# Performance work log

Hardware: AMD Instinct MI355X
Metric: run time of the kernel (lower is better)

The kernel has to match this reference:

```python
import jax, jax.numpy as jnp
import numpy as np

B, S, D, H = 2, 2048, 1024, 16
DH = D // H
LN_EPS = 1e-12


def setup_inputs() -> dict:
    key = jax.random.key(0)
    ks = jax.random.split(key, 11)
    s = 0.02
    return {
        "hidden_states": jax.random.normal(ks[0], (B, S, D), dtype=jnp.float32),
        "Wq": jax.random.normal(ks[1], (D, D), dtype=jnp.float32) * s,
        "bq": jnp.zeros((D,), jnp.float32),
        "Wk": jax.random.normal(ks[2], (D, D), dtype=jnp.float32) * s,
        "bk": jnp.zeros((D,), jnp.float32),
        "Wv": jax.random.normal(ks[3], (D, D), dtype=jnp.float32) * s,
        "bv": jnp.zeros((D,), jnp.float32),
        "Wd": jax.random.normal(ks[4], (D, D), dtype=jnp.float32) * s,  # torch Linear weight [out,in]
        "bd": jnp.zeros((D,), jnp.float32),
        "ln_g": jnp.ones((D,), jnp.float32),
        "ln_b": jnp.zeros((D,), jnp.float32),
    }


def reference(hidden_states, Wq, bq, Wk, bk, Wv, bv, Wd, bd, ln_g, ln_b):
    x = hidden_states  # [B,S,D]
    # torch Linear: y = x @ W.T + b
    def heads(y):
        return y.reshape(B, S, H, DH).transpose(0, 2, 1, 3)  # [B,H,S,DH]

    q = heads(x @ Wq.T + bq)
    k = heads(x @ Wk.T + bk)
    v = heads(x @ Wv.T + bv)

    scores = jnp.einsum('bhsd,bhtd->bhst', q, k) / jnp.sqrt(jnp.float32(DH))
    probs = jax.nn.softmax(scores, axis=-1)  # [B,H,S,S]
    ctx = jnp.einsum('bhst,bhtd->bshd', probs, v)  # [B,S,H,DH]

    # fused output projection: einsum('bfnd,ndh->bfh') with w = Wd.T reshaped
    w = Wd.T.reshape(H, DH, D)
    proj = jnp.einsum('bfnd,ndh->bfh', ctx, w) + bd  # [B,S,D]

    mu = jnp.mean(proj, axis=-1, keepdims=True)
    var = jnp.var(proj, axis=-1, keepdims=True)
    out = (proj - mu) / jnp.sqrt(var + LN_EPS) * ln_g + ln_b
    return out
```

## Files before the change

### kernel.cpp

```cpp
#include <hip/hip_runtime.h>

#define HD 16
#define DHEAD 64
#define DMODEL 1024
#define BB 2
#define SS 2048
#define MTOT (BB*SS)
#define LOG2E 1.44269504f

typedef float f32x4 __attribute__((ext_vector_type(4)));
typedef float f32x16 __attribute__((ext_vector_type(16)));
typedef __bf16 bf16x8 __attribute__((ext_vector_type(8)));
typedef unsigned short u16x8 __attribute__((ext_vector_type(8)));
typedef unsigned int u32x2 __attribute__((ext_vector_type(2)));
typedef unsigned int u32x4 __attribute__((ext_vector_type(4)));

__device__ __forceinline__ unsigned short f2bf(float f) {
    unsigned int u = __builtin_bit_cast(unsigned int, f);
    unsigned int r = (u + 0x7fffu + ((u >> 16) & 1u)) >> 16;
    return (unsigned short)r;
}

__device__ __forceinline__ bf16x8 ld8(const unsigned short* p) {
    u16x8 v = *reinterpret_cast<const u16x8*>(p);
    return __builtin_bit_cast(bf16x8, v);
}

__device__ __forceinline__ void gload_lds16b(const char* g, char* l) {
    __builtin_amdgcn_global_load_lds(
        (const __attribute__((address_space(1))) void*)g,
        (__attribute__((address_space(3))) void*)l, 16, 0, 0);
}

__device__ __forceinline__ unsigned cvt_pk_bf16(float lo, float hi) {
    unsigned r;
    asm("v_cvt_pk_bf16_f32 %0, %1, %2" : "=v"(r) : "v"(lo), "v"(hi));
    return r;
}

__global__ __launch_bounds__(256) void cvt_all(
    const float* __restrict__ x,
    const float* __restrict__ w0, const float* __restrict__ w1,
    const float* __restrict__ w2, const float* __restrict__ w3,
    unsigned short* __restrict__ xb,
    unsigned short* __restrict__ o0, unsigned short* __restrict__ o1,
    unsigned short* __restrict__ o2, unsigned short* __restrict__ o3) {
    int y = blockIdx.y;
    const float* in;
    unsigned short* out;
    int idx;
    if (y < 4) {
        in  = (y == 0) ? w0 : (y == 1) ? w1 : (y == 2) ? w2 : w3;
        out = (y == 0) ? o0 : (y == 1) ? o1 : (y == 2) ? o2 : o3;
        idx = blockIdx.x * 256 + threadIdx.x;
    } else {
        in  = x;
        out = xb;
        idx = ((y - 4) * 1024 + blockIdx.x) * 256 + threadIdx.x;
    }
    float4 v = reinterpret_cast<const float4*>(in)[idx];
    ushort4 o;
    o.x = f2bf(v.x); o.y = f2bf(v.y); o.z = f2bf(v.z); o.w = f2bf(v.w);
    reinterpret_cast<ushort4*>(out)[idx] = o;
}

__global__ __launch_bounds__(256, 2) void gemm_qkv(
    const unsigned short* __restrict__ xb,
    const unsigned short* __restrict__ Wqb, const unsigned short* __restrict__ Wkb,
    const unsigned short* __restrict__ Wvb,
    const float* __restrict__ bq, const float* __restrict__ bk, const float* __restrict__ bv,
    unsigned short* __restrict__ Qo, unsigned short* __restrict__ Ko, unsigned short* __restrict__ VTo) {
    __shared__ unsigned short Als[2][8192];
    __shared__ unsigned short Bls[2][8192];
    int L = blockIdx.x;
    int wg = (L & 7) * 96 + (L >> 3);
    int z = wg >> 8, rem = wg & 255;
    int n0 = (rem & 7) * 128, m0 = (rem >> 3) * 128;
    const unsigned short* Bm = (z == 0) ? Wqb : (z == 1) ? Wkb : Wvb;
    const float* bias = (z == 0) ? bq : (z == 1) ? bk : bv;

    int t = threadIdx.x, wv = t >> 6, lane = t & 63;
    int q5 = lane & 31, hi = lane >> 5;
    int wm = wv >> 1, wn = wv & 1;
    const char* Ac = (const char*)xb;
    const char* Bc = (const char*)Bm;

    auto stage = [&](int bf, int k0) {
#pragma unroll
        for (int i = 0; i < 4; ++i) {
            int c = t + 256 * i;
            int kr = c >> 3, kc = ((c & 7) << 4) ^ ((kr & 7) << 4);
            gload_lds16b(Ac + ((size_t)(m0 + kr) * DMODEL + k0) * 2 + kc, (char*)&Als[bf][0] + c * 16);
        }
#pragma unroll
        for (int i = 0; i < 4; ++i) {
            int c = t + 256 * i;
            int kr = c >> 3, kc = ((c & 7) << 4) ^ ((kr & 7) << 4);
            gload_lds16b(Bc + ((size_t)(n0 + kr) * DMODEL + k0) * 2 + kc, (char*)&Bls[bf][0] + c * 16);
        }
    };

    f32x16 acc[2][2];
#pragma unroll
    for (int fm = 0; fm < 2; ++fm)
#pragma unroll
        for (int fn = 0; fn < 2; ++fn) acc[fm][fn] = (f32x16)0.f;

    stage(0, 0);
    int buf = 0;
    for (int k0 = 0; k0 < DMODEL; k0 += 64) {
        __builtin_amdgcn_s_barrier();
        if (k0 + 64 < DMODEL) {
            stage(buf ^ 1, k0 + 64);
            asm volatile("s_waitcnt vmcnt(8)" ::: "memory");
        } else {
            asm volatile("s_waitcnt vmcnt(0)" ::: "memory");
        }
        __builtin_amdgcn_sched_barrier(0);
        __builtin_amdgcn_s_barrier();
        __builtin_amdgcn_sched_barrier(0);

        const char* als = (const char*)&Als[buf][0];
        const char* bls = (const char*)&Bls[buf][0];
        __builtin_amdgcn_s_setprio(1);
#pragma unroll
        for (int ks = 0; ks < 4; ++ks) {
            int kb = ks * 32 + hi * 16;
            bf16x8 af[2], bfr[2];
#pragma unroll
            for (int fm = 0; fm < 2; ++fm) {
                int row = wm * 64 + fm * 32 + q5;
                af[fm] = *reinterpret_cast<const bf16x8*>(als + row * 128 + (kb ^ ((row & 7) << 4)));
            }
#pragma unroll
            for (int fn = 0; fn < 2; ++fn) {
                int row = wn * 64 + fn * 32 + q5;
                bfr[fn] = *reinterpret_cast<const bf16x8*>(bls + row * 128 + (kb ^ ((row & 7) << 4)));
            }
#pragma unroll
            for (int fm = 0; fm < 2; ++fm)
#pragma unroll
                for (int fn = 0; fn < 2; ++fn)
                    acc[fm][fn] = __builtin_amdgcn_mfma_f32_32x32x16_bf16(af[fm], bfr[fn], acc[fm][fn], 0, 0, 0);
        }
        __builtin_amdgcn_s_setprio(0);
        buf ^= 1;
    }

    float scale = (z == 0) ? (0.125f * LOG2E) : 1.0f;
    int b = m0 >> 11;
#pragma unroll
    for (int fm = 0; fm < 2; ++fm) {
#pragma unroll
        for (int fn = 0; fn < 2; ++fn) {
            int col = n0 + wn * 64 + fn * 32 + q5;
            int h = col >> 6, dh = col & 63;
            float bi = bias[col];
            if (z == 2) {
#pragma unroll
                for (int rq = 0; rq < 4; ++rq) {
                    int s0 = ((m0 + wm * 64 + fm * 32 + 8 * rq + 4 * hi) & 2047);
                    ushort4 pk;
                    pk.x = f2bf(acc[fm][fn][4 * rq + 0] + bi);
                    pk.y = f2bf(acc[fm][fn][4 * rq + 1] + bi);
                    pk.z = f2bf(acc[fm][fn][4 * rq + 2] + bi);
                    pk.w = f2bf(acc[fm][fn][4 * rq + 3] + bi);
                    *reinterpret_cast<ushort4*>(&VTo[((size_t)((b * HD + h) * DHEAD + dh)) * SS + s0]) = pk;
                }
            } else {
                unsigned short* o = (z == 0) ? Qo : Ko;
#pragma unroll
                for (int r = 0; r < 16; ++r) {
                    int s = (m0 + wm * 64 + fm * 32 + (r & 3) + 8 * (r >> 2) + 4 * hi) & 2047;
                    o[((size_t)((b * HD + h) * SS + s)) * DHEAD + dh] = f2bf((acc[fm][fn][r] + bi) * scale);
                }
            }
        }
    }
}

__global__ __launch_bounds__(256, 2) void attn_kernel(
    const unsigned short* __restrict__ Qb, const unsigned short* __restrict__ Kb,
    const unsigned short* __restrict__ VTb, unsigned short* __restrict__ ctxo) {
    __shared__ unsigned short Kls[2][8192];
    __shared__ unsigned short Vls[2][8192];
    int L = blockIdx.x + (int)gridDim.x * blockIdx.y;
    int wg = (L & 7) * 64 + (L >> 3);
    int q0 = (wg & 15) * 128;
    int bh = wg >> 4;
    int t = threadIdx.x, wv = t >> 6, lane = t & 63;
    int q5 = lane & 31, hi = lane >> 5;
    const unsigned short* Qh  = Qb  + (size_t)bh * SS * DHEAD;
    const char* Khc  = (const char*)(Kb  + (size_t)bh * SS * DHEAD);
    const char* VThc = (const char*)(VTb + (size_t)bh * DHEAD * SS);
    int qr = q0 + wv * 32;

    bf16x8 qf[4];
#pragma unroll
    for (int m = 0; m < 4; ++m)
        qf[m] = ld8(&Qh[(size_t)(qr + q5) * DHEAD + m * 16 + hi * 8]);

    const __bf16 one_bf = (__bf16)1.0f;
    bf16x8 ones8 = {one_bf, one_bf, one_bf, one_bf, one_bf, one_bf, one_bf, one_bf};

    f32x16 oo[2];
    oo[0] = (f32x16)0.f; oo[1] = (f32x16)0.f;
    f32x16 ls = (f32x16)0.f;
    float mrun = 0.f;

    auto stage = [&](int buf, int t0) {
#pragma unroll
        for (int i = 0; i < 4; ++i) {
            int c = t + 256 * i;
            int kr = c >> 3, kc = ((c & 7) << 4) ^ ((kr & 7) << 4);
            gload_lds16b(Khc + (size_t)(t0 + kr) * 128 + kc, (char*)&Kls[buf][0] + c * 16);
        }
#pragma unroll
        for (int i = 0; i < 4; ++i) {
            int c = t + 256 * i;
            int vr = c >> 4, vc = ((c & 15) << 4) ^ ((vr & 7) << 4);
            gload_lds16b(VThc + ((size_t)vr * SS + t0) * 2 + vc, (char*)&Vls[buf][0] + c * 16);
        }
    };

    stage(0, 0);
    int buf = 0;

    for (int t0 = 0; t0 < SS; t0 += 128) {
        __builtin_amdgcn_s_barrier();
        if (t0 + 128 < SS) {
            stage(buf ^ 1, t0 + 128);
            asm volatile("s_waitcnt vmcnt(8)" ::: "memory");
        } else {
            asm volatile("s_waitcnt vmcnt(0)" ::: "memory");
        }
        __builtin_amdgcn_sched_barrier(0);
        __builtin_amdgcn_s_barrier();
        __builtin_amdgcn_sched_barrier(0);

        const char* kls = (const char*)&Kls[buf][0];
        const char* vls = (const char*)&Vls[buf][0];

#pragma unroll
        for (int half = 0; half < 2; ++half) {
            f32x16 sc[2];
            __builtin_amdgcn_s_setprio(1);
#pragma unroll
            for (int tb = 0; tb < 2; ++tb) {
                int row = (half * 2 + tb) * 32 + q5;
                int rsw = (row & 7) << 4;
                f32x16 s = (f32x16)0.f;
#pragma unroll
                for (int m = 0; m < 4; ++m) {
                    bf16x8 kf = *reinterpret_cast<const bf16x8*>(kls + row * 128 + ((m * 32 + hi * 16) ^ rsw));
                    s = __builtin_amdgcn_mfma_f32_32x32x16_bf16(kf, qf[m], s, 0, 0, 0);
                }
                sc[tb] = s;
            }
            __builtin_amdgcn_s_setprio(0);

            float mx[16];
#pragma unroll
            for (int r = 0; r < 16; ++r) mx[r] = fmaxf(sc[0][r], sc[1][r]);
#pragma unroll
            for (int st = 8; st; st >>= 1)
#pragma unroll
                for (int r = 0; r < st; ++r) mx[r] = fmaxf(mx[r], mx[r + st]);
            float lm = mx[0];

            if (__any(lm > mrun + 8.f)) {
                u32x2 sw = __builtin_amdgcn_permlane32_swap(__builtin_bit_cast(unsigned, lm),
                                                            __builtin_bit_cast(unsigned, lm), false, false);
                float rowmax = fmaxf(__builtin_bit_cast(float, sw[0]), __builtin_bit_cast(float, sw[1]));
                float mn = fmaxf(mrun, rowmax);
                float al = exp2f(mrun - mn);
                mrun = mn;
#pragma unroll
                for (int r = 0; r < 16; ++r) {
                    float alr = __shfl(al, (r & 3) + 8 * (r >> 2) + 4 * hi);
                    oo[0][r] *= alr; oo[1][r] *= alr; ls[r] *= alr;
                }
            }

#pragma unroll
            for (int tb = 0; tb < 2; ++tb)
#pragma unroll
                for (int r = 0; r < 16; ++r)
                    sc[tb][r] = exp2f(sc[tb][r] - mrun);

            u32x4 paw[4];
#pragma unroll
            for (int tb = 0; tb < 2; ++tb)
#pragma unroll
                for (int u2 = 0; u2 < 2; ++u2)
#pragma unroll
                    for (int e = 0; e < 2; ++e) {
                        unsigned wd = cvt_pk_bf16(sc[tb][8 * u2 + 2 * e], sc[tb][8 * u2 + 2 * e + 1]);
                        unsigned ws = cvt_pk_bf16(sc[tb][8 * u2 + 4 + 2 * e], sc[tb][8 * u2 + 4 + 2 * e + 1]);
                        u32x2 rr = __builtin_amdgcn_permlane32_swap(wd, ws, false, false);
                        paw[tb * 2 + u2][e] = rr[0];
                        paw[tb * 2 + u2][2 + e] = rr[1];
                    }

            __builtin_amdgcn_s_setprio(1);
#pragma unroll
            for (int dblk = 0; dblk < 2; ++dblk) {
                int row = dblk * 32 + q5;
                int rsw = (row & 7) << 4;
#pragma unroll
                for (int ks = 0; ks < 4; ++ks) {
                    bf16x8 vf = *reinterpret_cast<const bf16x8*>(
                        vls + row * 256 + ((half * 128 + ks * 32 + hi * 16) ^ rsw));
                    oo[dblk] = __builtin_amdgcn_mfma_f32_32x32x16_bf16(
                        __builtin_bit_cast(bf16x8, paw[ks]), vf, oo[dblk], 0, 0, 0);
                }
            }
#pragma unroll
            for (int ks = 0; ks < 4; ++ks)
                ls = __builtin_amdgcn_mfma_f32_32x32x16_bf16(
                    __builtin_bit_cast(bf16x8, paw[ks]), ones8, ls, 0, 0, 0);
            __builtin_amdgcn_s_setprio(0);
        }
        buf ^= 1;
    }

    int b = bh >> 4, h = bh & 15;
#pragma unroll
    for (int r = 0; r < 16; ++r) {
        float invr = 1.f / ls[r];
        int qrel = (r & 3) + 8 * (r >> 2) + 4 * hi;
        int s = qr + qrel;
        size_t base = ((size_t)(b * SS + s)) * DMODEL + h * DHEAD;
        ctxo[base + q5]      = f2bf(oo[0][r] * invr);
        ctxo[base + 32 + q5] = f2bf(oo[1][r] * invr);
    }
}

__global__ __launch_bounds__(256, 2) void gemm_proj(
    const unsigned short* __restrict__ ctxb, const unsigned short* __restrict__ Wdb,
    const float* __restrict__ bd, float* __restrict__ proj) {
    __shared__ unsigned short Als[2][8192];
    __shared__ unsigned short Bls[2][4096];
    int L = blockIdx.x;
    int wg = (L & 7) * 64 + (L >> 3);
    int n0 = (wg & 15) * 64, m0 = (wg >> 4) * 128;

    int t = threadIdx.x, wv = t >> 6, lane = t & 63;
    int q5 = lane & 31, hi = lane >> 5;
    int wm = wv >> 1, wn = wv & 1;
    const char* Ac = (const char*)ctxb;
    const char* Bc = (const char*)Wdb;

    auto stage = [&](int bf, int k0) {
#pragma unroll
        for (int i = 0; i < 4; ++i) {
            int c = t + 256 * i;
            int kr = c >> 3, kc = ((c & 7) << 4) ^ ((kr & 7) << 4);
            gload_lds16b(Ac + ((size_t)(m0 + kr) * DMODEL + k0) * 2 + kc, (char*)&Als[bf][0] + c * 16);
        }
#pragma unroll
        for (int i = 0; i < 2; ++i) {
            int c = t + 256 * i;
            int kr = c >> 3, kc = ((c & 7) << 4) ^ ((kr & 7) << 4);
            gload_lds16b(Bc + ((size_t)(n0 + kr) * DMODEL + k0) * 2 + kc, (char*)&Bls[bf][0] + c * 16);
        }
    };

    f32x16 acc[2];
    acc[0] = (f32x16)0.f; acc[1] = (f32x16)0.f;

    stage(0, 0);
    int buf = 0;
    for (int k0 = 0; k0 < DMODEL; k0 += 64) {
        __builtin_amdgcn_s_barrier();
        if (k0 + 64 < DMODEL) {
            stage(buf ^ 1, k0 + 64);
            asm volatile("s_waitcnt vmcnt(6)" ::: "memory");
        } else {
            asm volatile("s_waitcnt vmcnt(0)" ::: "memory");
        }
        __builtin_amdgcn_sched_barrier(0);
        __builtin_amdgcn_s_barrier();
        __builtin_amdgcn_sched_barrier(0);

        const char* als = (const char*)&Als[buf][0];
        const char* bls = (const char*)&Bls[buf][0];
        __builtin_amdgcn_s_setprio(1);
#pragma unroll
        for (int ks = 0; ks < 4; ++ks) {
            int kb = ks * 32 + hi * 16;
            bf16x8 af[2], bfr;
#pragma unroll
            for (int fm = 0; fm < 2; ++fm) {
                int row = wm * 64 + fm * 32 + q5;
                af[fm] = *reinterpret_cast<const bf16x8*>(als + row * 128 + (kb ^ ((row & 7) << 4)));
            }
            {
                int row = wn * 32 + q5;
                bfr = *reinterpret_cast<const bf16x8*>(bls + row * 128 + (kb ^ ((row & 7) << 4)));
            }
#pragma unroll
            for (int fm = 0; fm < 2; ++fm)
                acc[fm] = __builtin_amdgcn_mfma_f32_32x32x16_bf16(af[fm], bfr, acc[fm], 0, 0, 0);
        }
        __builtin_amdgcn_s_setprio(0);
        buf ^= 1;
    }

    int col = n0 + wn * 32 + q5;
    float bi = bd[col];
#pragma unroll
    for (int fm = 0; fm < 2; ++fm)
#pragma unroll
        for (int r = 0; r < 16; ++r) {
            int row = m0 + wm * 64 + fm * 32 + (r & 3) + 8 * (r >> 2) + 4 * hi;
            proj[(size_t)row * DMODEL + col] = acc[fm][r] + bi;
        }
}

__global__ __launch_bounds__(256) void ln_kernel(const float* __restrict__ proj,
                                                 const float* __restrict__ g,
                                                 const float* __restrict__ bv,
                                                 float* __restrict__ out) {
    int row = blockIdx.x, t = threadIdx.x;
    float4 v = reinterpret_cast<const float4*>(proj + (size_t)row * DMODEL)[t];
    float s  = v.x + v.y + v.z + v.w;
    float s2 = v.x * v.x + v.y * v.y + v.z * v.z + v.w * v.w;
#pragma unroll
    for (int m = 1; m < 64; m <<= 1) { s += __shfl_xor(s, m); s2 += __shfl_xor(s2, m); }
    __shared__ float red[8];
    int wv = t >> 6, lane = t & 63;
    if (lane == 0) { red[wv] = s; red[wv + 4] = s2; }
    __syncthreads();
    s  = red[0] + red[1] + red[2] + red[3];
    s2 = red[4] + red[5] + red[6] + red[7];
    float mu  = s * (1.f / 1024.f);
    float var = s2 * (1.f / 1024.f) - mu * mu;
    float inv = rsqrtf(var + 1e-12f);
    float4 gv = reinterpret_cast<const float4*>(g)[t];
    float4 bb = reinterpret_cast<const float4*>(bv)[t];
    float4 ov;
    ov.x = (v.x - mu) * inv * gv.x + bb.x;
    ov.y = (v.y - mu) * inv * gv.y + bb.y;
    ov.z = (v.z - mu) * inv * gv.z + bb.z;
    ov.w = (v.w - mu) * inv * gv.w + bb.w;
    reinterpret_cast<float4*>(out + (size_t)row * DMODEL)[t] = ov;
}

extern "C" void kernel_launch(void* const* d_in, const int* in_sizes, int n_in,
                              void* d_out, int out_size, void* d_ws, size_t ws_size,
                              hipStream_t stream) {
    const float* x   = (const float*)d_in[0];
    const float* Wq  = (const float*)d_in[1];
    const float* bq  = (const float*)d_in[2];
    const float* Wk  = (const float*)d_in[3];
    const float* bk  = (const float*)d_in[4];
    const float* Wv  = (const float*)d_in[5];
    const float* bv  = (const float*)d_in[6];
    const float* Wd  = (const float*)d_in[7];
    const float* bd  = (const float*)d_in[8];
    const float* lng = (const float*)d_in[9];
    const float* lnb = (const float*)d_in[10];

    char* ws = (char*)d_ws;
    unsigned short* xb   = (unsigned short*)(ws);
    unsigned short* Wqb  = (unsigned short*)(ws + (8u  << 20));
    unsigned short* Wkb  = (unsigned short*)(ws + (10u << 20));
    unsigned short* Wvb  = (unsigned short*)(ws + (12u << 20));
    unsigned short* Wdb  = (unsigned short*)(ws + (14u << 20));
    unsigned short* Qb   = (unsigned short*)(ws + (16u << 20));
    unsigned short* Kb   = (unsigned short*)(ws + (24u << 20));
    unsigned short* VTb  = (unsigned short*)(ws + (32u << 20));
    unsigned short* ctxb = (unsigned short*)(ws + (40u << 20));
    float* proj = (float*)(ws + (16u << 20));

    cvt_all<<<dim3(1024, 8), 256, 0, stream>>>(x, Wq, Wk, Wv, Wd, xb, Wqb, Wkb, Wvb, Wdb);
    gemm_qkv<<<768, 256, 0, stream>>>(xb, Wqb, Wkb, Wvb, bq, bk, bv, Qb, Kb, VTb);
    attn_kernel<<<dim3(16, 32), 256, 0, stream>>>(Qb, Kb, VTb, ctxb);
    gemm_proj<<<512, 256, 0, stream>>>(ctxb, Wdb, bd, proj);
    ln_kernel<<<4096, 256, 0, stream>>>(proj, lng, lnb, (float*)d_out);
}
```

Measured before the change: 140.4 us.

## Split attention key tiles across two wave groups and merge partial softmax states

The attention block grows from 256 to 512 threads. Two groups of four waves each take one half of every 128-key tile for the same 32 query rows. At the end, the second group writes its partial output, row sum and running max to LDS, and the first group rescales and merges both before writing ctx. This doubles the waves in flight to hide MFMA and exp latency, at the cost of a final LDS merge, extra barriers and launch_bounds(512,4) register pressure.

```diff
diff --git a/kernel.cpp b/kernel.cpp
--- a/kernel.cpp
+++ b/kernel.cpp
@@ -179,21 +179,21 @@
     }
 }
 
-__global__ __launch_bounds__(256, 2) void attn_kernel(
+__global__ __launch_bounds__(512, 4) void attn_kernel(
     const unsigned short* __restrict__ Qb, const unsigned short* __restrict__ Kb,
     const unsigned short* __restrict__ VTb, unsigned short* __restrict__ ctxo) {
-    __shared__ unsigned short Kls[2][8192];
-    __shared__ unsigned short Vls[2][8192];
+    __shared__ char smem[65536];
     int L = blockIdx.x + (int)gridDim.x * blockIdx.y;
     int wg = (L & 7) * 64 + (L >> 3);
     int q0 = (wg & 15) * 128;
     int bh = wg >> 4;
     int t = threadIdx.x, wv = t >> 6, lane = t & 63;
+    int g = wv & 3, hf = wv >> 2;
     int q5 = lane & 31, hi = lane >> 5;
     const unsigned short* Qh  = Qb  + (size_t)bh * SS * DHEAD;
     const char* Khc  = (const char*)(Kb  + (size_t)bh * SS * DHEAD);
     const char* VThc = (const char*)(VTb + (size_t)bh * DHEAD * SS);
-    int qr = q0 + wv * 32;
+    int qr = q0 + g * 32;
 
     bf16x8 qf[4];
 #pragma unroll
@@ -209,17 +209,19 @@
     float mrun = 0.f;
 
     auto stage = [&](int buf, int t0) {
-#pragma unroll
-        for (int i = 0; i < 4; ++i) {
-            int c = t + 256 * i;
+        char* kb = smem + buf * 32768;
+        char* vb = kb + 16384;
+#pragma unroll
+        for (int i = 0; i < 2; ++i) {
+            int c = t + 512 * i;
             int kr = c >> 3, kc = ((c & 7) << 4) ^ ((kr & 7) << 4);
-            gload_lds16b(Khc + (size_t)(t0 + kr) * 128 + kc, (char*)&Kls[buf][0] + c * 16);
-        }
-#pragma unroll
-        for (int i = 0; i < 4; ++i) {
-            int c = t + 256 * i;
+            gload_lds16b(Khc + (size_t)(t0 + kr) * 128 + kc, kb + c * 16);
+        }
+#pragma unroll
+        for (int i = 0; i < 2; ++i) {
+            int c = t + 512 * i;
             int vr = c >> 4, vc = ((c & 15) << 4) ^ ((vr & 7) << 4);
-            gload_lds16b(VThc + ((size_t)vr * SS + t0) * 2 + vc, (char*)&Vls[buf][0] + c * 16);
+            gload_lds16b(VThc + ((size_t)vr * SS + t0) * 2 + vc, vb + c * 16);
         }
     };
 
@@ -230,7 +232,7 @@
         __builtin_amdgcn_s_barrier();
         if (t0 + 128 < SS) {
             stage(buf ^ 1, t0 + 128);
-            asm volatile("s_waitcnt vmcnt(8)" ::: "memory");
+            asm volatile("s_waitcnt vmcnt(4)" ::: "memory");
         } else {
             asm volatile("s_waitcnt vmcnt(0)" ::: "memory");
         }
@@ -238,101 +240,124 @@
         __builtin_amdgcn_s_barrier();
         __builtin_amdgcn_sched_barrier(0);
 
-        const char* kls = (const char*)&Kls[buf][0];
-        const char* vls = (const char*)&Vls[buf][0];
-
-#pragma unroll
-        for (int half = 0; half < 2; ++half) {
-            f32x16 sc[2];
-            __builtin_amdgcn_s_setprio(1);
-#pragma unroll
-            for (int tb = 0; tb < 2; ++tb) {
-                int row = (half * 2 + tb) * 32 + q5;
-                int rsw = (row & 7) << 4;
-                f32x16 s = (f32x16)0.f;
-#pragma unroll
-                for (int m = 0; m < 4; ++m) {
-                    bf16x8 kf = *reinterpret_cast<const bf16x8*>(kls + row * 128 + ((m * 32 + hi * 16) ^ rsw));
-                    s = __builtin_amdgcn_mfma_f32_32x32x16_bf16(kf, qf[m], s, 0, 0, 0);
+        const char* kls = smem + buf * 32768;
+        const char* vls = kls + 16384;
+
+        f32x16 sc[2];
+        __builtin_amdgcn_s_setprio(1);
+#pragma unroll
+        for (int tb = 0; tb < 2; ++tb) {
+            int row = hf * 64 + tb * 32 + q5;
+            int rsw = (row & 7) << 4;
+            f32x16 s = (f32x16)0.f;
+#pragma unroll
+            for (int m = 0; m < 4; ++m) {
+                bf16x8 kf = *reinterpret_cast<const bf16x8*>(kls + row * 128 + ((m * 32 + hi * 16) ^ rsw));
+                s = __builtin_amdgcn_mfma_f32_32x32x16_bf16(kf, qf[m], s, 0, 0, 0);
+            }
+            sc[tb] = s;
+        }
+        __builtin_amdgcn_s_setprio(0);
+
+        float mx[16];
+#pragma unroll
+        for (int r = 0; r < 16; ++r) mx[r] = fmaxf(sc[0][r], sc[1][r]);
+#pragma unroll
+        for (int st = 8; st; st >>= 1)
+#pragma unroll
+            for (int r = 0; r < st; ++r) mx[r] = fmaxf(mx[r], mx[r + st]);
+        float lm = mx[0];
+
+        if (__any(lm > mrun + 8.f)) {
+            u32x2 sw = __builtin_amdgcn_permlane32_swap(__builtin_bit_cast(unsigned, lm),
+                                                        __builtin_bit_cast(unsigned, lm), false, false);
+            float rowmax = fmaxf(__builtin_bit_cast(float, sw[0]), __builtin_bit_cast(float, sw[1]));
+            float mn = fmaxf(mrun, rowmax);
+            float al = exp2f(mrun - mn);
+            mrun = mn;
+#pragma unroll
+            for (int r = 0; r < 16; ++r) {
+                float alr = __shfl(al, (r & 3) + 8 * (r >> 2) + 4 * hi);
+                oo[0][r] *= alr; oo[1][r] *= alr; ls[r] *= alr;
+            }
+        }
+
+#pragma unroll
+        for (int tb = 0; tb < 2; ++tb)
+#pragma unroll
+            for (int r = 0; r < 16; ++r)
+                sc[tb][r] = exp2f(sc[tb][r] - mrun);
+
+        u32x4 paw[4];
+#pragma unroll
+        for (int tb = 0; tb < 2; ++tb)
+#pragma unroll
+            for (int u2 = 0; u2 < 2; ++u2)
+#pragma unroll
+                for (int e = 0; e < 2; ++e) {
+                    unsigned wd = cvt_pk_bf16(sc[tb][8 * u2 + 2 * e], sc[tb][8 * u2 + 2 * e + 1]);
+                    unsigned ws = cvt_pk_bf16(sc[tb][8 * u2 + 4 + 2 * e], sc[tb][8 * u2 + 4 + 2 * e + 1]);
+                    u32x2 rr = __builtin_amdgcn_permlane32_swap(wd, ws, false, false);
+                    paw[tb * 2 + u2][e] = rr[0];
+                    paw[tb * 2 + u2][2 + e] = rr[1];
                 }
-                sc[tb] = s;
-            }
-            __builtin_amdgcn_s_setprio(0);
-
-            float mx[16];
-#pragma unroll
-            for (int r = 0; r < 16; ++r) mx[r] = fmaxf(sc[0][r], sc[1][r]);
-#pragma unroll
-            for (int st = 8; st; st >>= 1)
-#pragma unroll
-                for (int r = 0; r < st; ++r) mx[r] = fmaxf(mx[r], mx[r + st]);
-            float lm = mx[0];
-
-            if (__any(lm > mrun + 8.f)) {
-                u32x2 sw = __builtin_amdgcn_permlane32_swap(__builtin_bit_cast(unsigned, lm),
-                                                            __builtin_bit_cast(unsigned, lm), false, false);
-                float rowmax = fmaxf(__builtin_bit_cast(float, sw[0]), __builtin_bit_cast(float, sw[1]));
-                float mn = fmaxf(mrun, rowmax);
-                float al = exp2f(mrun - mn);
-                mrun = mn;
-#pragma unroll
-                for (int r = 0; r < 16; ++r) {
-                    float alr = __shfl(al, (r & 3) + 8 * (r >> 2) + 4 * hi);
-                    oo[0][r] *= alr; oo[1][r] *= alr; ls[r] *= alr;
-                }
-            }
-
-#pragma unroll
-            for (int tb = 0; tb < 2; ++tb)
-#pragma unroll
-                for (int r = 0; r < 16; ++r)
-                    sc[tb][r] = exp2f(sc[tb][r] - mrun);
-
-            u32x4 paw[4];
-#pragma unroll
-            for (int tb = 0; tb < 2; ++tb)
-#pragma unroll
-                for (int u2 = 0; u2 < 2; ++u2)
-#pragma unroll
-                    for (int e = 0; e < 2; ++e) {
-                        unsigned wd = cvt_pk_bf16(sc[tb][8 * u2 + 2 * e], sc[tb][8 * u2 + 2 * e + 1]);
-                        unsigned ws = cvt_pk_bf16(sc[tb][8 * u2 + 4 + 2 * e], sc[tb][8 * u2 + 4 + 2 * e + 1]);
-                        u32x2 rr = __builtin_amdgcn_permlane32_swap(wd, ws, false, false);
-                        paw[tb * 2 + u2][e] = rr[0];
-                        paw[tb * 2 + u2][2 + e] = rr[1];
-                    }
-
-            __builtin_amdgcn_s_setprio(1);
-#pragma unroll
-            for (int dblk = 0; dblk < 2; ++dblk) {
-                int row = dblk * 32 + q5;
-                int rsw = (row & 7) << 4;
-#pragma unroll
-                for (int ks = 0; ks < 4; ++ks) {
-                    bf16x8 vf = *reinterpret_cast<const bf16x8*>(
-                        vls + row * 256 + ((half * 128 + ks * 32 + hi * 16) ^ rsw));
-                    oo[dblk] = __builtin_amdgcn_mfma_f32_32x32x16_bf16(
-                        __builtin_bit_cast(bf16x8, paw[ks]), vf, oo[dblk], 0, 0, 0);
-                }
-            }
-#pragma unroll
-            for (int ks = 0; ks < 4; ++ks)
-                ls = __builtin_amdgcn_mfma_f32_32x32x16_bf16(
-                    __builtin_bit_cast(bf16x8, paw[ks]), ones8, ls, 0, 0, 0);
-            __builtin_amdgcn_s_setprio(0);
-        }
+
+        __builtin_amdgcn_s_setprio(1);
+#pragma unroll
+        for (int dblk = 0; dblk < 2; ++dblk) {
+            int row = dblk * 32 + q5;
+            int rsw = (row & 7) << 4;
+#pragma unroll
+            for (int ks = 0; ks < 4; ++ks) {
+                bf16x8 vf = *reinterpret_cast<const bf16x8*>(
+                    vls + row * 256 + ((hf * 128 + ks * 32 + hi * 16) ^ rsw));
+                oo[dblk] = __builtin_amdgcn_mfma_f32_32x32x16_bf16(
+                    __builtin_bit_cast(bf16x8, paw[ks]), vf, oo[dblk], 0, 0, 0);
+            }
+        }
+#pragma unroll
+        for (int ks = 0; ks < 4; ++ks)
+            ls = __builtin_amdgcn_mfma_f32_32x32x16_bf16(
+                __builtin_bit_cast(bf16x8, paw[ks]), ones8, ls, 0, 0, 0);
+        __builtin_amdgcn_s_setprio(0);
         buf ^= 1;
     }
 
-    int b = bh >> 4, h = bh & 15;
-#pragma unroll
-    for (int r = 0; r < 16; ++r) {
-        float invr = 1.f / ls[r];
-        int qrel = (r & 3) + 8 * (r >> 2) + 4 * hi;
-        int s = qr + qrel;
-        size_t base = ((size_t)(b * SS + s)) * DMODEL + h * DHEAD;
-        ctxo[base + q5]      = f2bf(oo[0][r] * invr);
-        ctxo[base + 32 + q5] = f2bf(oo[1][r] * invr);
+    __builtin_amdgcn_s_barrier();
+    float* mb = (float*)smem;
+    int mbase = (g * 64 + lane) * 52;
+    if (hf) {
+#pragma unroll
+        for (int r = 0; r < 16; ++r) {
+            mb[mbase + r]      = oo[0][r];
+            mb[mbase + 16 + r] = oo[1][r];
+            mb[mbase + 32 + r] = ls[r];
+        }
+        mb[mbase + 48] = mrun;
+    }
+    __builtin_amdgcn_s_barrier();
+    if (!hf) {
+        float mbv = mb[mbase + 48];
+        int b = bh >> 4, h = bh & 15;
+#pragma unroll
+        for (int r = 0; r < 16; ++r) {
+            int qrel = (r & 3) + 8 * (r >> 2) + 4 * hi;
+            float ma = __shfl(mrun, qrel);
+            float mbq = __shfl(mbv, qrel);
+            float mm = fmaxf(ma, mbq);
+            float sa = exp2f(ma - mm), sb = exp2f(mbq - mm);
+            float ob0 = mb[mbase + r];
+            float ob1 = mb[mbase + 16 + r];
+            float lb  = mb[mbase + 32 + r];
+            float l = ls[r] * sa + lb * sb;
+            float inv = 1.f / l;
+            float o0 = (oo[0][r] * sa + ob0 * sb) * inv;
+            float o1 = (oo[1][r] * sa + ob1 * sb) * inv;
+            int s = qr + qrel;
+            size_t base = ((size_t)(b * SS + s)) * DMODEL + h * DHEAD;
+            ctxo[base + q5]      = f2bf(o0);
+            ctxo[base + 32 + q5] = f2bf(o1);
+        }
     }
 }
 
@@ -476,7 +501,7 @@
 
     cvt_all<<<dim3(1024, 8), 256, 0, stream>>>(x, Wq, Wk, Wv, Wd, xb, Wqb, Wkb, Wvb, Wdb);
     gemm_qkv<<<768, 256, 0, stream>>>(xb, Wqb, Wkb, Wvb, bq, bk, bv, Qb, Kb, VTb);
-    attn_kernel<<<dim3(16, 32), 256, 0, stream>>>(Qb, Kb, VTb, ctxb);
+    attn_kernel<<<dim3(16, 32), 512, 0, stream>>>(Qb, Kb, VTb, ctxb);
     gemm_proj<<<512, 256, 0, stream>>>(ctxb, Wdb, bd, proj);
     ln_kernel<<<4096, 256, 0, stream>>>(proj, lng, lnb, (float*)d_out);
 }
```

Result: slower. 148.3 us (+5.7%).
